# Kernel optimization log

Hardware: AMD Instinct MI355X
Metric: run time of the kernel (lower is better)

The kernel has to match this reference:

```python
import jax, jax.numpy as jnp
import numpy as np

N = 50000      # nodes
E = 800000     # directed edges (before self-loops)
FEAT = 120     # raw node feature dim
TOPO = 8       # topological feature dim
H1, D1 = 8, 8  # conv1: heads, per-head dim
C = 40         # out_channels (classes)
NEG_SLOPE = 0.2


def setup_inputs() -> dict:
    key = jax.random.key(0)
    ks = jax.random.split(key, 10)
    return {
        "x": jax.random.normal(ks[0], (N, FEAT), dtype=jnp.float32),
        "topo": jax.random.normal(ks[1], (N, TOPO), dtype=jnp.float32),
        "edge_index": jax.random.randint(ks[2], (2, E), 0, N, dtype=jnp.int32),
        "W1": jax.random.normal(ks[3], (FEAT + TOPO, H1 * D1), dtype=jnp.float32) * 0.1,
        "a_src1": jax.random.normal(ks[4], (H1, D1), dtype=jnp.float32) * 0.1,
        "a_dst1": jax.random.normal(ks[5], (H1, D1), dtype=jnp.float32) * 0.1,
        "b1": jnp.zeros((H1 * D1,), dtype=jnp.float32),
        "W2": jax.random.normal(ks[6], (H1 * D1, C), dtype=jnp.float32) * 0.1,
        "a_src2": jax.random.normal(ks[7], (1, C), dtype=jnp.float32) * 0.1,
        "a_dst2": jax.random.normal(ks[8], (1, C), dtype=jnp.float32) * 0.1,
        "b2": jnp.zeros((C,), dtype=jnp.float32),
    }


def gat_conv(x, src, dst, W, a_src, a_dst, b, heads, d, concat):
    """PyG-style GATConv (eval mode). src/dst already include self-loops."""
    n = x.shape[0]
    h = (x @ W).reshape(n, heads, d)                      # [N,H,D]
    al_src = jnp.sum(h * a_src[None], axis=-1)            # [N,H]
    al_dst = jnp.sum(h * a_dst[None], axis=-1)            # [N,H]
    e = jax.nn.leaky_relu(al_src[src] + al_dst[dst], NEG_SLOPE)  # [E',H]
    # segment softmax over incoming edges per destination node
    m = jax.ops.segment_max(e, dst, num_segments=n)       # [N,H]
    p = jnp.exp(e - m[dst])                               # [E',H]
    s = jax.ops.segment_sum(p, dst, num_segments=n)       # [N,H]
    alpha = p / s[dst]                                    # [E',H]
    out = jax.ops.segment_sum(alpha[:, :, None] * h[src], dst, num_segments=n)  # [N,H,D]
    if concat:
        return out.reshape(n, heads * d) + b
    return out.mean(axis=1) + b


def reference(x, topo, edge_index, W1, a_src1, a_dst1, b1, W2, a_src2, a_dst2, b2):
    n = x.shape[0]
    loops = jnp.arange(n, dtype=edge_index.dtype)
    src = jnp.concatenate([edge_index[0], loops])
    dst = jnp.concatenate([edge_index[1], loops])
    xin = jnp.concatenate([x, topo], axis=1)              # [N, FEAT+TOPO]
    h = jax.nn.elu(gat_conv(xin, src, dst, W1, a_src1, a_dst1, b1, H1, D1, True))
    out = gat_conv(h, src, dst, W2, a_src2, a_dst2, b2, 1, C, False)
    return jax.nn.log_softmax(out, axis=1)
```

## Files before the change

kernel.cpp:

```cpp
#include <hip/hip_runtime.h>
#include <hip/hip_fp16.h>

#define NN 50000
#define EE 800000
#define ET 850000
#define NBUCK 196
#define CAP 5120
#define TILEA 2048
#define NBA ((EE + TILEA - 1) / TILEA)
#define NGB 782

typedef _Float16 half8 __attribute__((ext_vector_type(8)));
typedef float floatx4 __attribute__((ext_vector_type(4)));

__global__ void k_zero(int* __restrict__ c) {
    int i = threadIdx.x;
    if (i < NBUCK) c[i] = 0;
}

__global__ __launch_bounds__(256) void k_bucketA(const int* __restrict__ ei,
        int* __restrict__ cursor, unsigned* __restrict__ bucketData) {
    __shared__ int cnt[NBUCK], base[NBUCK];
    int t = threadIdx.x;
    for (int i = t; i < NBUCK; i += 256) cnt[i] = 0;
    __syncthreads();
    int e0 = blockIdx.x * TILEA;
    int nE = min(TILEA, EE - e0);
    unsigned pk[8]; int bk[8], rk[8];
    int m = 0;
    for (int i = t; i < nE; i += 256) {
        int e = e0 + i;
        int s = ei[e], d = ei[EE + e];
        pk[m] = ((unsigned)d << 16) | (unsigned)s;
        bk[m] = d >> 8;
        rk[m] = atomicAdd(&cnt[bk[m]], 1);
        m++;
    }
    __syncthreads();
    for (int i = t; i < NBUCK; i += 256)
        base[i] = (cnt[i] > 0) ? atomicAdd(&cursor[i], cnt[i]) : 0;
    __syncthreads();
    for (int k = 0; k < m; k++) {
        int pos = base[bk[k]] + rk[k];
        if (pos < CAP) bucketData[(size_t)bk[k] * CAP + pos] = pk[k];
    }
}

__global__ void k_scanB(const int* __restrict__ cursor, int* __restrict__ bucketOut,
                        int* __restrict__ rowstart) {
    __shared__ int s0[256], s1[256];
    int t = threadIdx.x;
    int nloc = (t < NBUCK) ? min(256, NN - t * 256) : 0;
    int v = (t < NBUCK) ? (min(cursor[t], CAP) + nloc) : 0;
    s0[t] = v;
    __syncthreads();
    int* a = s0; int* b = s1;
    for (int off = 1; off < 256; off <<= 1) {
        int x = a[t] + ((t >= off) ? a[t - off] : 0);
        b[t] = x;
        __syncthreads();
        int* tmp = a; a = b; b = tmp;
    }
    if (t < NBUCK) bucketOut[t] = a[t] - v;
    if (t == NBUCK - 1) rowstart[NN] = a[t];
}

__global__ __launch_bounds__(256) void k_bucketB(const unsigned* __restrict__ bucketData,
        const int* __restrict__ cursor, const int* __restrict__ bucketOut,
        int* __restrict__ rowstart, int* __restrict__ srcs) {
    __shared__ int cnt[256], cur[256], sbuf[256];
    __shared__ int sorted[CAP + 256];
    int b = blockIdx.x, t = threadIdx.x;
    int nloc = min(256, NN - b * 256);
    int ecnt = min(cursor[b], CAP);
    size_t inBase = (size_t)b * CAP;
    int outBase = bucketOut[b];
    cnt[t] = (t < nloc) ? 1 : 0;
    __syncthreads();
    for (int i = t; i < ecnt; i += 256) {
        unsigned u = bucketData[inBase + i];
        atomicAdd(&cnt[(u >> 16) & 255], 1);
    }
    __syncthreads();
    int cv = cnt[t];
    sbuf[t] = cv;
    __syncthreads();
    int* a = sbuf; int* bb = cnt;
    for (int off = 1; off < 256; off <<= 1) {
        int x = a[t] + ((t >= off) ? a[t - off] : 0);
        bb[t] = x;
        __syncthreads();
        int* tmp = a; a = bb; bb = tmp;
    }
    int excl = a[t] - cv;
    __syncthreads();
    if (t < nloc) {
        rowstart[b * 256 + t] = outBase + excl;
        sorted[excl] = b * 256 + t;
        cur[t] = excl + 1;
    } else {
        cur[t] = 0;
    }
    __syncthreads();
    for (int i = t; i < ecnt; i += 256) {
        unsigned u = bucketData[inBase + i];
        int ld = (u >> 16) & 255;
        int p = atomicAdd(&cur[ld], 1);
        sorted[p] = (int)(u & 0xffffu);
    }
    __syncthreads();
    int total = ecnt + nloc;
    for (int i = t; i < total; i += 256) srcs[outBase + i] = sorted[i];
}

__global__ void k_prep(const float* __restrict__ W1, const float* __restrict__ W2,
                       _Float16* __restrict__ Bf1, _Float16* __restrict__ Bf2) {
    int tid = blockIdx.x * 256 + threadIdx.x;
    if (tid < 1024) {
        int kk = tid >> 8, ct = (tid >> 6) & 3, L = tid & 63;
        int k0 = kk * 32 + (L >> 4) * 8, col = ct * 16 + (L & 15);
        half8 v;
        #pragma unroll
        for (int j = 0; j < 8; j++) v[j] = (_Float16)W1[(k0 + j) * 64 + col];
        *(half8*)(Bf1 + ((size_t)((kk * 4 + ct) * 64 + L)) * 8) = v;
    } else if (tid < 1024 + 384) {
        int u = tid - 1024;
        int kk = u / 192, rem = u % 192;
        int ct = rem >> 6, L = rem & 63;
        int k0 = kk * 32 + (L >> 4) * 8, col = ct * 16 + (L & 15);
        half8 v;
        #pragma unroll
        for (int j = 0; j < 8; j++)
            v[j] = (col < 40) ? (_Float16)W2[(k0 + j) * 40 + col] : (_Float16)0.f;
        *(half8*)(Bf2 + ((size_t)((kk * 3 + ct) * 64 + L)) * 8) = v;
    }
}

__global__ __launch_bounds__(256) void k_gemm1(
    const float* __restrict__ x, const float* __restrict__ topo,
    const _Float16* __restrict__ Bf1,
    const float* __restrict__ a_src, const float* __restrict__ a_dst,
    __half* __restrict__ h1, float* __restrict__ alsrc, float* __restrict__ aldst) {
    int wave = threadIdx.x >> 6, lane = threadIdx.x & 63;
    int row0 = blockIdx.x * 64 + wave * 16;
    if (row0 >= NN) return;
    int g = lane >> 4, li = lane & 15;
    int myrow = row0 + li;
    half8 B[16];
    const half8* bp = (const half8*)Bf1;
    #pragma unroll
    for (int i = 0; i < 16; i++) B[i] = bp[i * 64 + lane];
    floatx4 acc[4] = {{0,0,0,0},{0,0,0,0},{0,0,0,0},{0,0,0,0}};
    #pragma unroll
    for (int kk = 0; kk < 4; kk++) {
        int k0 = kk * 32 + g * 8;
        const float* sp = (k0 == 120) ? (topo + (size_t)myrow * 8)
                                      : (x + (size_t)myrow * 120 + k0);
        float4 u0 = ((const float4*)sp)[0];
        float4 u1 = ((const float4*)sp)[1];
        half8 av;
        av[0] = (_Float16)u0.x; av[1] = (_Float16)u0.y;
        av[2] = (_Float16)u0.z; av[3] = (_Float16)u0.w;
        av[4] = (_Float16)u1.x; av[5] = (_Float16)u1.y;
        av[6] = (_Float16)u1.z; av[7] = (_Float16)u1.w;
        #pragma unroll
        for (int ct = 0; ct < 4; ct++)
            acc[ct] = __builtin_amdgcn_mfma_f32_16x16x32_f16(av, B[kk * 4 + ct], acc[ct], 0, 0, 0);
    }
    #pragma unroll
    for (int ct = 0; ct < 4; ct++)
        #pragma unroll
        for (int r = 0; r < 4; r++)
            h1[(size_t)(row0 + 4 * g + r) * 64 + ct * 16 + li] = __float2half(acc[ct][r]);
    float ps[4][4], pd[4][4];
    #pragma unroll
    for (int ct = 0; ct < 4; ct++) {
        int head = 2 * ct + (li >> 3), dix = li & 7;
        float asv = a_src[head * 8 + dix];
        float adv = a_dst[head * 8 + dix];
        #pragma unroll
        for (int r = 0; r < 4; r++) {
            ps[ct][r] = acc[ct][r] * asv;
            pd[ct][r] = acc[ct][r] * adv;
        }
    }
    #pragma unroll
    for (int off = 1; off <= 4; off <<= 1)
        #pragma unroll
        for (int ct = 0; ct < 4; ct++)
            #pragma unroll
            for (int r = 0; r < 4; r++) {
                ps[ct][r] += __shfl_xor(ps[ct][r], off, 64);
                pd[ct][r] += __shfl_xor(pd[ct][r], off, 64);
            }
    if ((li & 7) == 0) {
        #pragma unroll
        for (int ct = 0; ct < 4; ct++) {
            int head = 2 * ct + (li >> 3);
            #pragma unroll
            for (int r = 0; r < 4; r++) {
                int row = row0 + 4 * g + r;
                alsrc[row * 8 + head] = ps[ct][r];
                aldst[row * 8 + head] = pd[ct][r];
            }
        }
    }
}

__global__ __launch_bounds__(256) void k_agg1(
    const int* __restrict__ rowstart, const int* __restrict__ srcs,
    const float* __restrict__ alsrc, const float* __restrict__ aldst,
    const __half* __restrict__ h1, const float* __restrict__ b1,
    __half* __restrict__ hout) {
    int wave = threadIdx.x >> 6;
    int lane = threadIdx.x & 63;
    int d = blockIdx.x * 4 + wave;
    if (d >= NN) return;
    int half = lane >> 5;
    int cp = lane & 31;
    int h = cp >> 2;
    float adst = aldst[d * 8 + h];
    int jb = rowstart[d], je = rowstart[d + 1];
    float ssum = 0.f;
    float ax = 0.f, ay = 0.f;
    int j = jb;
    for (; j + 8 <= je; j += 8) {
        int s0 = srcs[j + half], s1 = srcs[j + 2 + half];
        int s2 = srcs[j + 4 + half], s3 = srcs[j + 6 + half];
        float e0 = alsrc[s0 * 8 + h] + adst;
        float e1 = alsrc[s1 * 8 + h] + adst;
        float e2 = alsrc[s2 * 8 + h] + adst;
        float e3 = alsrc[s3 * 8 + h] + adst;
        __half2 v0 = *(const __half2*)(h1 + (size_t)s0 * 64 + 2 * cp);
        __half2 v1 = *(const __half2*)(h1 + (size_t)s1 * 64 + 2 * cp);
        __half2 v2 = *(const __half2*)(h1 + (size_t)s2 * 64 + 2 * cp);
        __half2 v3 = *(const __half2*)(h1 + (size_t)s3 * 64 + 2 * cp);
        float p0 = __expf(fmaxf(e0, 0.2f * e0));
        float p1 = __expf(fmaxf(e1, 0.2f * e1));
        float p2 = __expf(fmaxf(e2, 0.2f * e2));
        float p3 = __expf(fmaxf(e3, 0.2f * e3));
        float2 f0 = __half22float2(v0), f1 = __half22float2(v1);
        float2 f2 = __half22float2(v2), f3 = __half22float2(v3);
        ssum += (p0 + p1) + (p2 + p3);
        ax += p0 * f0.x + p1 * f1.x + p2 * f2.x + p3 * f3.x;
        ay += p0 * f0.y + p1 * f1.y + p2 * f2.y + p3 * f3.y;
    }
    for (; j < je; j += 2) {
        int e = j + half;
        bool valid = (e < je);
        int s = srcs[valid ? e : jb];
        float ea = alsrc[s * 8 + h] + adst;
        float p = valid ? __expf(fmaxf(ea, 0.2f * ea)) : 0.f;
        float2 f = __half22float2(*(const __half2*)(h1 + (size_t)s * 64 + 2 * cp));
        ssum += p;
        ax += p * f.x;
        ay += p * f.y;
    }
    ssum += __shfl_xor(ssum, 32, 64);
    ax += __shfl_xor(ax, 32, 64);
    ay += __shfl_xor(ay, 32, 64);
    if (half == 0) {
        float2 bv = *(const float2*)(b1 + 2 * cp);
        float inv = 1.f / ssum;
        float vx = ax * inv + bv.x;
        float vy = ay * inv + bv.y;
        vx = (vx > 0.f) ? vx : (__expf(vx) - 1.f);
        vy = (vy > 0.f) ? vy : (__expf(vy) - 1.f);
        *(__half2*)(hout + (size_t)d * 64 + 2 * cp) = __floats2half2_rn(vx, vy);
    }
}

__global__ __launch_bounds__(256) void k_gemm2(
    const __half* __restrict__ hout, const _Float16* __restrict__ Bf2,
    const float* __restrict__ a_src2, const float* __restrict__ a_dst2,
    __half* __restrict__ h2, float* __restrict__ al2s, float* __restrict__ al2d) {
    int wave = threadIdx.x >> 6, lane = threadIdx.x & 63;
    int row0 = blockIdx.x * 64 + wave * 16;
    if (row0 >= NN) return;
    int g = lane >> 4, li = lane & 15;
    int myrow = row0 + li;
    half8 B[6];
    const half8* bp = (const half8*)Bf2;
    #pragma unroll
    for (int i = 0; i < 6; i++) B[i] = bp[i * 64 + lane];
    floatx4 acc[3] = {{0,0,0,0},{0,0,0,0},{0,0,0,0}};
    #pragma unroll
    for (int kk = 0; kk < 2; kk++) {
        int k0 = kk * 32 + g * 8;
        half8 av = *(const half8*)(hout + (size_t)myrow * 64 + k0);
        #pragma unroll
        for (int ct = 0; ct < 3; ct++)
            acc[ct] = __builtin_amdgcn_mfma_f32_16x16x32_f16(av, B[kk * 3 + ct], acc[ct], 0, 0, 0);
    }
    float ts[4] = {0.f, 0.f, 0.f, 0.f}, td[4] = {0.f, 0.f, 0.f, 0.f};
    #pragma unroll
    for (int ct = 0; ct < 3; ct++) {
        int col = ct * 16 + li;
        bool ok = (col < 40);
        float asv = ok ? a_src2[col] : 0.f;
        float adv = ok ? a_dst2[col] : 0.f;
        #pragma unroll
        for (int r = 0; r < 4; r++) {
            ts[r] += acc[ct][r] * asv;
            td[r] += acc[ct][r] * adv;
            if (ok) h2[(size_t)(row0 + 4 * g + r) * 40 + col] = __float2half(acc[ct][r]);
        }
    }
    #pragma unroll
    for (int off = 1; off <= 8; off <<= 1)
        #pragma unroll
        for (int r = 0; r < 4; r++) {
            ts[r] += __shfl_xor(ts[r], off, 64);
            td[r] += __shfl_xor(td[r], off, 64);
        }
    if (li == 0) {
        #pragma unroll
        for (int r = 0; r < 4; r++) {
            int row = row0 + 4 * g + r;
            al2s[row] = ts[r];
            al2d[row] = td[r];
        }
    }
}

__global__ __launch_bounds__(256) void k_agg2(
    const int* __restrict__ rowstart, const int* __restrict__ srcs,
    const float* __restrict__ al2s, const float* __restrict__ al2d,
    const __half* __restrict__ h2, const float* __restrict__ b2,
    float* __restrict__ out) {
    int wave = threadIdx.x >> 6;
    int lane = threadIdx.x & 63;
    int d = blockIdx.x * 4 + wave;
    if (d >= NN) return;
    int half = lane >> 5;
    int cp = lane & 31;
    bool act = (cp < 20);
    int cpc = act ? cp : 0;
    float adst = al2d[d];
    int jb = rowstart[d], je = rowstart[d + 1];
    float ssum = 0.f, ax = 0.f, ay = 0.f;
    int j = jb;
    for (; j + 8 <= je; j += 8) {
        int s0 = srcs[j + half], s1 = srcs[j + 2 + half];
        int s2 = srcs[j + 4 + half], s3 = srcs[j + 6 + half];
        float e0 = al2s[s0] + adst;
        float e1 = al2s[s1] + adst;
        float e2 = al2s[s2] + adst;
        float e3 = al2s[s3] + adst;
        __half2 v0 = *(const __half2*)(h2 + (size_t)s0 * 40 + 2 * cpc);
        __half2 v1 = *(const __half2*)(h2 + (size_t)s1 * 40 + 2 * cpc);
        __half2 v2 = *(const __half2*)(h2 + (size_t)s2 * 40 + 2 * cpc);
        __half2 v3 = *(const __half2*)(h2 + (size_t)s3 * 40 + 2 * cpc);
        float p0 = __expf(fmaxf(e0, 0.2f * e0));
        float p1 = __expf(fmaxf(e1, 0.2f * e1));
        float p2 = __expf(fmaxf(e2, 0.2f * e2));
        float p3 = __expf(fmaxf(e3, 0.2f * e3));
        float2 f0 = __half22float2(v0), f1 = __half22float2(v1);
        float2 f2 = __half22float2(v2), f3 = __half22float2(v3);
        ssum += (p0 + p1) + (p2 + p3);
        ax += p0 * f0.x + p1 * f1.x + p2 * f2.x + p3 * f3.x;
        ay += p0 * f0.y + p1 * f1.y + p2 * f2.y + p3 * f3.y;
    }
    for (; j < je; j += 2) {
        int e = j + half;
        bool valid = (e < je);
        int s = srcs[valid ? e : jb];
        float ea = al2s[s] + adst;
        float p = valid ? __expf(fmaxf(ea, 0.2f * ea)) : 0.f;
        float2 f = __half22float2(*(const __half2*)(h2 + (size_t)s * 40 + 2 * cpc));
        ssum += p;
        ax += p * f.x;
        ay += p * f.y;
    }
    ssum += __shfl_xor(ssum, 32, 64);
    ax += __shfl_xor(ax, 32, 64);
    ay += __shfl_xor(ay, 32, 64);
    float inv = 1.f / ssum;
    float2 bv = *(const float2*)(b2 + 2 * cpc);
    float ox = ax * inv + bv.x;
    float oy = ay * inv + bv.y;
    float mo = act ? fmaxf(ox, oy) : -3.0e38f;
    #pragma unroll
    for (int off = 16; off; off >>= 1) mo = fmaxf(mo, __shfl_xor(mo, off, 64));
    float te = act ? (__expf(ox - mo) + __expf(oy - mo)) : 0.f;
    #pragma unroll
    for (int off = 16; off; off >>= 1) te += __shfl_xor(te, off, 64);
    float ls = __logf(te);
    if (act && half == 0)
        *(float2*)(out + (size_t)d * 40 + 2 * cp) = make_float2(ox - mo - ls, oy - mo - ls);
}

extern "C" void kernel_launch(void* const* d_in, const int* in_sizes, int n_in,
                              void* d_out, int out_size, void* d_ws, size_t ws_size,
                              hipStream_t stream) {
    (void)in_sizes; (void)n_in; (void)out_size; (void)ws_size;
    const float* x    = (const float*)d_in[0];
    const float* topo = (const float*)d_in[1];
    const int*   ei   = (const int*)d_in[2];
    const float* W1   = (const float*)d_in[3];
    const float* as1  = (const float*)d_in[4];
    const float* ad1  = (const float*)d_in[5];
    const float* b1   = (const float*)d_in[6];
    const float* W2   = (const float*)d_in[7];
    const float* as2  = (const float*)d_in[8];
    const float* ad2  = (const float*)d_in[9];
    const float* b2   = (const float*)d_in[10];
    float* out = (float*)d_out;

    char* ws = (char*)d_ws;
    size_t off = 0;
    auto alloc = [&](size_t bytes) {
        void* p = ws + off;
        off += (bytes + 255) / 256 * 256;
        return p;
    };
    int*       rowstart   = (int*)alloc((NN + 1) * 4);
    int*       cursor     = (int*)alloc(NBUCK * 4);
    int*       bucketOut  = (int*)alloc(NBUCK * 4);
    unsigned*  bucketData = (unsigned*)alloc((size_t)NBUCK * CAP * 4);
    int*       srcs       = (int*)alloc(ET * 4);
    float*     alsrc1     = (float*)alloc((size_t)NN * 8 * 4);
    float*     aldst1     = (float*)alloc((size_t)NN * 8 * 4);
    float*     al2s       = (float*)alloc(NN * 4);
    float*     al2d       = (float*)alloc(NN * 4);
    _Float16*  Bf1        = (_Float16*)alloc(4 * 4 * 64 * 8 * 2);
    _Float16*  Bf2        = (_Float16*)alloc(2 * 3 * 64 * 8 * 2);
    __half*    h1         = (__half*)alloc((size_t)NN * 64 * 2);
    __half*    hout       = (__half*)alloc((size_t)NN * 64 * 2);
    __half*    h2         = h1;

    k_zero    <<<1,     256, 0, stream>>>(cursor);
    k_prep    <<<6,     256, 0, stream>>>(W1, W2, Bf1, Bf2);
    k_bucketA <<<NBA,   256, 0, stream>>>(ei, cursor, bucketData);
    k_scanB   <<<1,     256, 0, stream>>>(cursor, bucketOut, rowstart);
    k_bucketB <<<NBUCK, 256, 0, stream>>>(bucketData, cursor, bucketOut, rowstart, srcs);
    k_gemm1   <<<NGB,   256, 0, stream>>>(x, topo, Bf1, as1, ad1, h1, alsrc1, aldst1);
    k_agg1    <<<(NN + 3) / 4, 256, 0, stream>>>(rowstart, srcs, alsrc1, aldst1, h1, b1, hout);
    k_gemm2   <<<NGB,   256, 0, stream>>>(hout, Bf2, as2, ad2, h2, al2s, al2d);
    k_agg2    <<<(NN + 3) / 4, 256, 0, stream>>>(rowstart, srcs, al2s, al2d, h2, b2, out);
}
```

Before: 204.3 us.

## Fuse layer-2 GEMM into aggregation, pad CSR rows to multiples of 8

```diff
diff --git a/kernel.cpp b/kernel.cpp
--- a/kernel.cpp
+++ b/kernel.cpp
@@ -3,19 +3,33 @@
 
 #define NN 50000
 #define EE 800000
-#define ET 850000
 #define NBUCK 196
 #define CAP 5120
-#define TILEA 2048
+#define TILEA 1024
 #define NBA ((EE + TILEA - 1) / TILEA)
 #define NGB 782
+#define SRCS_MAX (EE + 8 * NN)
 
 typedef _Float16 half8 __attribute__((ext_vector_type(8)));
 typedef float floatx4 __attribute__((ext_vector_type(4)));
 
-__global__ void k_zero(int* __restrict__ c) {
-    int i = threadIdx.x;
-    if (i < NBUCK) c[i] = 0;
+__global__ void k_prep(const float* __restrict__ W1, _Float16* __restrict__ Bf1,
+                       int* __restrict__ cursor, float* __restrict__ alsrc,
+                       float* __restrict__ al2s) {
+    int tid = blockIdx.x * 256 + threadIdx.x;
+    if (tid < 1024) {
+        int kk = tid >> 8, ct = (tid >> 6) & 3, L = tid & 63;
+        int k0 = kk * 32 + (L >> 4) * 8, col = ct * 16 + (L & 15);
+        half8 v;
+        #pragma unroll
+        for (int j = 0; j < 8; j++) v[j] = (_Float16)W1[(k0 + j) * 64 + col];
+        *(half8*)(Bf1 + ((size_t)((kk * 4 + ct) * 64 + L)) * 8) = v;
+    } else {
+        int u = tid - 1024;
+        if (u < NBUCK) cursor[u] = 0;
+        if (u >= 200 && u < 208) alsrc[(size_t)NN * 8 + (u - 200)] = -1e30f;
+        if (u == 208) al2s[NN] = -1e30f;
+    }
 }
 
 __global__ __launch_bounds__(256) void k_bucketA(const int* __restrict__ ei,
@@ -26,7 +40,7 @@
     __syncthreads();
     int e0 = blockIdx.x * TILEA;
     int nE = min(TILEA, EE - e0);
-    unsigned pk[8]; int bk[8], rk[8];
+    unsigned pk[4]; int bk[4], rk[4];
     int m = 0;
     for (int i = t; i < nE; i += 256) {
         int e = e0 + i;
@@ -46,12 +60,11 @@
     }
 }
 
-__global__ void k_scanB(const int* __restrict__ cursor, int* __restrict__ bucketOut,
-                        int* __restrict__ rowstart) {
+__global__ void k_scanB(const int* __restrict__ cursor, int* __restrict__ bucketOut) {
     __shared__ int s0[256], s1[256];
     int t = threadIdx.x;
     int nloc = (t < NBUCK) ? min(256, NN - t * 256) : 0;
-    int v = (t < NBUCK) ? (min(cursor[t], CAP) + nloc) : 0;
+    int v = (t < NBUCK) ? (min(cursor[t], CAP) + 8 * nloc) : 0;
     s0[t] = v;
     __syncthreads();
     int* a = s0; int* b = s1;
@@ -62,14 +75,13 @@
         int* tmp = a; a = b; b = tmp;
     }
     if (t < NBUCK) bucketOut[t] = a[t] - v;
-    if (t == NBUCK - 1) rowstart[NN] = a[t];
 }
 
 __global__ __launch_bounds__(256) void k_bucketB(const unsigned* __restrict__ bucketData,
         const int* __restrict__ cursor, const int* __restrict__ bucketOut,
-        int* __restrict__ rowstart, int* __restrict__ srcs) {
+        int2* __restrict__ rowseg, int* __restrict__ srcs) {
     __shared__ int cnt[256], cur[256], sbuf[256];
-    __shared__ int sorted[CAP + 256];
+    __shared__ int sorted[CAP + 2048];
     int b = blockIdx.x, t = threadIdx.x;
     int nloc = min(256, NN - b * 256);
     int ecnt = min(cursor[b], CAP);
@@ -83,7 +95,8 @@
     }
     __syncthreads();
     int cv = cnt[t];
-    sbuf[t] = cv;
+    int pcv = (t < nloc) ? ((cv + 7) & ~7) : 0;
+    sbuf[t] = pcv;
     __syncthreads();
     int* a = sbuf; int* bb = cnt;
     for (int off = 1; off < 256; off <<= 1) {
@@ -92,14 +105,14 @@
         __syncthreads();
         int* tmp = a; a = bb; bb = tmp;
     }
-    int excl = a[t] - cv;
+    int excl = a[t] - pcv;
+    int total = a[255];
     __syncthreads();
     if (t < nloc) {
-        rowstart[b * 256 + t] = outBase + excl;
+        rowseg[b * 256 + t] = make_int2(outBase + excl, outBase + excl + pcv);
         sorted[excl] = b * 256 + t;
+        for (int k = cv; k < pcv; k++) sorted[excl + k] = NN;
         cur[t] = excl + 1;
-    } else {
-        cur[t] = 0;
     }
     __syncthreads();
     for (int i = t; i < ecnt; i += 256) {
@@ -109,31 +122,7 @@
         sorted[p] = (int)(u & 0xffffu);
     }
     __syncthreads();
-    int total = ecnt + nloc;
     for (int i = t; i < total; i += 256) srcs[outBase + i] = sorted[i];
-}
-
-__global__ void k_prep(const float* __restrict__ W1, const float* __restrict__ W2,
-                       _Float16* __restrict__ Bf1, _Float16* __restrict__ Bf2) {
-    int tid = blockIdx.x * 256 + threadIdx.x;
-    if (tid < 1024) {
-        int kk = tid >> 8, ct = (tid >> 6) & 3, L = tid & 63;
-        int k0 = kk * 32 + (L >> 4) * 8, col = ct * 16 + (L & 15);
-        half8 v;
-        #pragma unroll
-        for (int j = 0; j < 8; j++) v[j] = (_Float16)W1[(k0 + j) * 64 + col];
-        *(half8*)(Bf1 + ((size_t)((kk * 4 + ct) * 64 + L)) * 8) = v;
-    } else if (tid < 1024 + 384) {
-        int u = tid - 1024;
-        int kk = u / 192, rem = u % 192;
-        int ct = rem >> 6, L = rem & 63;
-        int k0 = kk * 32 + (L >> 4) * 8, col = ct * 16 + (L & 15);
-        half8 v;
-        #pragma unroll
-        for (int j = 0; j < 8; j++)
-            v[j] = (col < 40) ? (_Float16)W2[(k0 + j) * 40 + col] : (_Float16)0.f;
-        *(half8*)(Bf2 + ((size_t)((kk * 3 + ct) * 64 + L)) * 8) = v;
-    }
 }
 
 __global__ __launch_bounds__(256) void k_gemm1(
@@ -208,186 +197,149 @@
 }
 
 __global__ __launch_bounds__(256) void k_agg1(
-    const int* __restrict__ rowstart, const int* __restrict__ srcs,
+    const int2* __restrict__ rowseg, const int* __restrict__ srcs,
     const float* __restrict__ alsrc, const float* __restrict__ aldst,
     const __half* __restrict__ h1, const float* __restrict__ b1,
-    __half* __restrict__ hout) {
-    int wave = threadIdx.x >> 6;
-    int lane = threadIdx.x & 63;
-    int d = blockIdx.x * 4 + wave;
-    if (d >= NN) return;
-    int half = lane >> 5;
+    const float* __restrict__ W2, const float* __restrict__ as2g,
+    const float* __restrict__ ad2g,
+    __half* __restrict__ h2, float* __restrict__ al2s, float* __restrict__ al2d) {
+    __shared__ float W2s[64 * 40];
+    __shared__ float as2s[40], ad2s[40];
+    int t = threadIdx.x;
+    for (int i = t; i < 2560; i += 256) W2s[i] = W2[i];
+    if (t < 40) { as2s[t] = as2g[t]; ad2s[t] = ad2g[t]; }
+    __syncthreads();
+    int wave = t >> 6, lane = t & 63;
+    int hs = lane >> 5;
     int cp = lane & 31;
-    int h = cp >> 2;
-    float adst = aldst[d * 8 + h];
-    int jb = rowstart[d], je = rowstart[d + 1];
-    float ssum = 0.f;
-    float ax = 0.f, ay = 0.f;
-    int j = jb;
-    for (; j + 8 <= je; j += 8) {
-        int s0 = srcs[j + half], s1 = srcs[j + 2 + half];
-        int s2 = srcs[j + 4 + half], s3 = srcs[j + 6 + half];
-        float e0 = alsrc[s0 * 8 + h] + adst;
-        float e1 = alsrc[s1 * 8 + h] + adst;
-        float e2 = alsrc[s2 * 8 + h] + adst;
-        float e3 = alsrc[s3 * 8 + h] + adst;
-        __half2 v0 = *(const __half2*)(h1 + (size_t)s0 * 64 + 2 * cp);
-        __half2 v1 = *(const __half2*)(h1 + (size_t)s1 * 64 + 2 * cp);
-        __half2 v2 = *(const __half2*)(h1 + (size_t)s2 * 64 + 2 * cp);
-        __half2 v3 = *(const __half2*)(h1 + (size_t)s3 * 64 + 2 * cp);
-        float p0 = __expf(fmaxf(e0, 0.2f * e0));
-        float p1 = __expf(fmaxf(e1, 0.2f * e1));
-        float p2 = __expf(fmaxf(e2, 0.2f * e2));
-        float p3 = __expf(fmaxf(e3, 0.2f * e3));
-        float2 f0 = __half22float2(v0), f1 = __half22float2(v1);
-        float2 f2 = __half22float2(v2), f3 = __half22float2(v3);
-        ssum += (p0 + p1) + (p2 + p3);
-        ax += p0 * f0.x + p1 * f1.x + p2 * f2.x + p3 * f3.x;
-        ay += p0 * f0.y + p1 * f1.y + p2 * f2.y + p3 * f3.y;
-    }
-    for (; j < je; j += 2) {
-        int e = j + half;
-        bool valid = (e < je);
-        int s = srcs[valid ? e : jb];
-        float ea = alsrc[s * 8 + h] + adst;
-        float p = valid ? __expf(fmaxf(ea, 0.2f * ea)) : 0.f;
-        float2 f = __half22float2(*(const __half2*)(h1 + (size_t)s * 64 + 2 * cp));
-        ssum += p;
-        ax += p * f.x;
-        ay += p * f.y;
-    }
-    ssum += __shfl_xor(ssum, 32, 64);
-    ax += __shfl_xor(ax, 32, 64);
-    ay += __shfl_xor(ay, 32, 64);
-    if (half == 0) {
+    int hh = cp >> 2;
+    int c = lane;
+    bool ok = (c < 40);
+    int cc = ok ? c : 0;
+    for (int g = 0; g < 4; g++) {
+        int d = blockIdx.x * 16 + wave * 4 + g;
+        int2 seg = rowseg[d];
+        int jb = seg.x, je = seg.y;
+        float adst = aldst[d * 8 + hh];
+        float ssum = 0.f, ax = 0.f, ay = 0.f;
+        int sA0 = srcs[jb + hs],     sA1 = srcs[jb + 2 + hs];
+        int sA2 = srcs[jb + 4 + hs], sA3 = srcs[jb + 6 + hs];
+        for (int j = jb; j < je; j += 8) {
+            int s0 = sA0, s1 = sA1, s2 = sA2, s3 = sA3;
+            int jn = j + 8;
+            if (jn < je) {
+                sA0 = srcs[jn + hs];     sA1 = srcs[jn + 2 + hs];
+                sA2 = srcs[jn + 4 + hs]; sA3 = srcs[jn + 6 + hs];
+            }
+            float e0 = alsrc[s0 * 8 + hh] + adst;
+            float e1 = alsrc[s1 * 8 + hh] + adst;
+            float e2 = alsrc[s2 * 8 + hh] + adst;
+            float e3 = alsrc[s3 * 8 + hh] + adst;
+            __half2 v0 = *(const __half2*)(h1 + (size_t)s0 * 64 + 2 * cp);
+            __half2 v1 = *(const __half2*)(h1 + (size_t)s1 * 64 + 2 * cp);
+            __half2 v2 = *(const __half2*)(h1 + (size_t)s2 * 64 + 2 * cp);
+            __half2 v3 = *(const __half2*)(h1 + (size_t)s3 * 64 + 2 * cp);
+            float p0 = __expf(fmaxf(e0, 0.2f * e0));
+            float p1 = __expf(fmaxf(e1, 0.2f * e1));
+            float p2 = __expf(fmaxf(e2, 0.2f * e2));
+            float p3 = __expf(fmaxf(e3, 0.2f * e3));
+            float2 f0 = __half22float2(v0), f1 = __half22float2(v1);
+            float2 f2 = __half22float2(v2), f3 = __half22float2(v3);
+            ssum += (p0 + p1) + (p2 + p3);
+            ax += p0 * f0.x + p1 * f1.x + p2 * f2.x + p3 * f3.x;
+            ay += p0 * f0.y + p1 * f1.y + p2 * f2.y + p3 * f3.y;
+        }
+        ssum += __shfl_xor(ssum, 32, 64);
+        ax += __shfl_xor(ax, 32, 64);
+        ay += __shfl_xor(ay, 32, 64);
         float2 bv = *(const float2*)(b1 + 2 * cp);
         float inv = 1.f / ssum;
-        float vx = ax * inv + bv.x;
-        float vy = ay * inv + bv.y;
-        vx = (vx > 0.f) ? vx : (__expf(vx) - 1.f);
-        vy = (vy > 0.f) ? vy : (__expf(vy) - 1.f);
-        *(__half2*)(hout + (size_t)d * 64 + 2 * cp) = __floats2half2_rn(vx, vy);
-    }
-}
-
-__global__ __launch_bounds__(256) void k_gemm2(
-    const __half* __restrict__ hout, const _Float16* __restrict__ Bf2,
-    const float* __restrict__ a_src2, const float* __restrict__ a_dst2,
-    __half* __restrict__ h2, float* __restrict__ al2s, float* __restrict__ al2d) {
-    int wave = threadIdx.x >> 6, lane = threadIdx.x & 63;
-    int row0 = blockIdx.x * 64 + wave * 16;
-    if (row0 >= NN) return;
-    int g = lane >> 4, li = lane & 15;
-    int myrow = row0 + li;
-    half8 B[6];
-    const half8* bp = (const half8*)Bf2;
-    #pragma unroll
-    for (int i = 0; i < 6; i++) B[i] = bp[i * 64 + lane];
-    floatx4 acc[3] = {{0,0,0,0},{0,0,0,0},{0,0,0,0}};
-    #pragma unroll
-    for (int kk = 0; kk < 2; kk++) {
-        int k0 = kk * 32 + g * 8;
-        half8 av = *(const half8*)(hout + (size_t)myrow * 64 + k0);
-        #pragma unroll
-        for (int ct = 0; ct < 3; ct++)
-            acc[ct] = __builtin_amdgcn_mfma_f32_16x16x32_f16(av, B[kk * 3 + ct], acc[ct], 0, 0, 0);
-    }
-    float ts[4] = {0.f, 0.f, 0.f, 0.f}, td[4] = {0.f, 0.f, 0.f, 0.f};
-    #pragma unroll
-    for (int ct = 0; ct < 3; ct++) {
-        int col = ct * 16 + li;
-        bool ok = (col < 40);
-        float asv = ok ? a_src2[col] : 0.f;
-        float adv = ok ? a_dst2[col] : 0.f;
-        #pragma unroll
-        for (int r = 0; r < 4; r++) {
-            ts[r] += acc[ct][r] * asv;
-            td[r] += acc[ct][r] * adv;
-            if (ok) h2[(size_t)(row0 + 4 * g + r) * 40 + col] = __float2half(acc[ct][r]);
-        }
-    }
-    #pragma unroll
-    for (int off = 1; off <= 8; off <<= 1)
-        #pragma unroll
-        for (int r = 0; r < 4; r++) {
-            ts[r] += __shfl_xor(ts[r], off, 64);
-            td[r] += __shfl_xor(td[r], off, 64);
-        }
-    if (li == 0) {
-        #pragma unroll
-        for (int r = 0; r < 4; r++) {
-            int row = row0 + 4 * g + r;
-            al2s[row] = ts[r];
-            al2d[row] = td[r];
-        }
+        float hx = ax * inv + bv.x;
+        float hy = ay * inv + bv.y;
+        hx = (hx > 0.f) ? hx : (__expf(hx) - 1.f);
+        hy = (hy > 0.f) ? hy : (__expf(hy) - 1.f);
+        float o = 0.f;
+        #pragma unroll
+        for (int kp = 0; kp < 32; kp++) {
+            float hxk = __shfl(hx, kp, 64);
+            float hyk = __shfl(hy, kp, 64);
+            o += hxk * W2s[(2 * kp) * 40 + cc] + hyk * W2s[(2 * kp + 1) * 40 + cc];
+        }
+        float s1v = ok ? o * as2s[cc] : 0.f;
+        float s2v = ok ? o * ad2s[cc] : 0.f;
+        #pragma unroll
+        for (int off = 1; off <= 32; off <<= 1) {
+            s1v += __shfl_xor(s1v, off, 64);
+            s2v += __shfl_xor(s2v, off, 64);
+        }
+        if (lane == 0) { al2s[d] = s1v; al2d[d] = s2v; }
+        float oN = __shfl(o, lane + 1, 64);
+        if (ok && !(c & 1))
+            *(__half2*)(h2 + (size_t)d * 40 + c) = __floats2half2_rn(o, oN);
     }
 }
 
 __global__ __launch_bounds__(256) void k_agg2(
-    const int* __restrict__ rowstart, const int* __restrict__ srcs,
+    const int2* __restrict__ rowseg, const int* __restrict__ srcs,
     const float* __restrict__ al2s, const float* __restrict__ al2d,
     const __half* __restrict__ h2, const float* __restrict__ b2,
     float* __restrict__ out) {
     int wave = threadIdx.x >> 6;
     int lane = threadIdx.x & 63;
-    int d = blockIdx.x * 4 + wave;
-    if (d >= NN) return;
-    int half = lane >> 5;
+    int hs = lane >> 5;
     int cp = lane & 31;
     bool act = (cp < 20);
     int cpc = act ? cp : 0;
-    float adst = al2d[d];
-    int jb = rowstart[d], je = rowstart[d + 1];
-    float ssum = 0.f, ax = 0.f, ay = 0.f;
-    int j = jb;
-    for (; j + 8 <= je; j += 8) {
-        int s0 = srcs[j + half], s1 = srcs[j + 2 + half];
-        int s2 = srcs[j + 4 + half], s3 = srcs[j + 6 + half];
-        float e0 = al2s[s0] + adst;
-        float e1 = al2s[s1] + adst;
-        float e2 = al2s[s2] + adst;
-        float e3 = al2s[s3] + adst;
-        __half2 v0 = *(const __half2*)(h2 + (size_t)s0 * 40 + 2 * cpc);
-        __half2 v1 = *(const __half2*)(h2 + (size_t)s1 * 40 + 2 * cpc);
-        __half2 v2 = *(const __half2*)(h2 + (size_t)s2 * 40 + 2 * cpc);
-        __half2 v3 = *(const __half2*)(h2 + (size_t)s3 * 40 + 2 * cpc);
-        float p0 = __expf(fmaxf(e0, 0.2f * e0));
-        float p1 = __expf(fmaxf(e1, 0.2f * e1));
-        float p2 = __expf(fmaxf(e2, 0.2f * e2));
-        float p3 = __expf(fmaxf(e3, 0.2f * e3));
-        float2 f0 = __half22float2(v0), f1 = __half22float2(v1);
-        float2 f2 = __half22float2(v2), f3 = __half22float2(v3);
-        ssum += (p0 + p1) + (p2 + p3);
-        ax += p0 * f0.x + p1 * f1.x + p2 * f2.x + p3 * f3.x;
-        ay += p0 * f0.y + p1 * f1.y + p2 * f2.y + p3 * f3.y;
-    }
-    for (; j < je; j += 2) {
-        int e = j + half;
-        bool valid = (e < je);
-        int s = srcs[valid ? e : jb];
-        float ea = al2s[s] + adst;
-        float p = valid ? __expf(fmaxf(ea, 0.2f * ea)) : 0.f;
-        float2 f = __half22float2(*(const __half2*)(h2 + (size_t)s * 40 + 2 * cpc));
-        ssum += p;
-        ax += p * f.x;
-        ay += p * f.y;
-    }
-    ssum += __shfl_xor(ssum, 32, 64);
-    ax += __shfl_xor(ax, 32, 64);
-    ay += __shfl_xor(ay, 32, 64);
-    float inv = 1.f / ssum;
-    float2 bv = *(const float2*)(b2 + 2 * cpc);
-    float ox = ax * inv + bv.x;
-    float oy = ay * inv + bv.y;
-    float mo = act ? fmaxf(ox, oy) : -3.0e38f;
-    #pragma unroll
-    for (int off = 16; off; off >>= 1) mo = fmaxf(mo, __shfl_xor(mo, off, 64));
-    float te = act ? (__expf(ox - mo) + __expf(oy - mo)) : 0.f;
-    #pragma unroll
-    for (int off = 16; off; off >>= 1) te += __shfl_xor(te, off, 64);
-    float ls = __logf(te);
-    if (act && half == 0)
-        *(float2*)(out + (size_t)d * 40 + 2 * cp) = make_float2(ox - mo - ls, oy - mo - ls);
+    for (int g = 0; g < 4; g++) {
+        int d = blockIdx.x * 16 + wave * 4 + g;
+        int2 seg = rowseg[d];
+        int jb = seg.x, je = seg.y;
+        float adst = al2d[d];
+        float ssum = 0.f, ax = 0.f, ay = 0.f;
+        int sA0 = srcs[jb + hs],     sA1 = srcs[jb + 2 + hs];
+        int sA2 = srcs[jb + 4 + hs], sA3 = srcs[jb + 6 + hs];
+        for (int j = jb; j < je; j += 8) {
+            int s0 = sA0, s1 = sA1, s2 = sA2, s3 = sA3;
+            int jn = j + 8;
+            if (jn < je) {
+                sA0 = srcs[jn + hs];     sA1 = srcs[jn + 2 + hs];
+                sA2 = srcs[jn + 4 + hs]; sA3 = srcs[jn + 6 + hs];
+            }
+            float e0 = al2s[s0] + adst;
+            float e1 = al2s[s1] + adst;
+            float e2 = al2s[s2] + adst;
+            float e3 = al2s[s3] + adst;
+            __half2 v0 = *(const __half2*)(h2 + (size_t)s0 * 40 + 2 * cpc);
+            __half2 v1 = *(const __half2*)(h2 + (size_t)s1 * 40 + 2 * cpc);
+            __half2 v2 = *(const __half2*)(h2 + (size_t)s2 * 40 + 2 * cpc);
+            __half2 v3 = *(const __half2*)(h2 + (size_t)s3 * 40 + 2 * cpc);
+            float p0 = __expf(fmaxf(e0, 0.2f * e0));
+            float p1 = __expf(fmaxf(e1, 0.2f * e1));
+            float p2 = __expf(fmaxf(e2, 0.2f * e2));
+            float p3 = __expf(fmaxf(e3, 0.2f * e3));
+            float2 f0 = __half22float2(v0), f1 = __half22float2(v1);
+            float2 f2 = __half22float2(v2), f3 = __half22float2(v3);
+            ssum += (p0 + p1) + (p2 + p3);
+            ax += p0 * f0.x + p1 * f1.x + p2 * f2.x + p3 * f3.x;
+            ay += p0 * f0.y + p1 * f1.y + p2 * f2.y + p3 * f3.y;
+        }
+        ssum += __shfl_xor(ssum, 32, 64);
+        ax += __shfl_xor(ax, 32, 64);
+        ay += __shfl_xor(ay, 32, 64);
+        float inv = 1.f / ssum;
+        float2 bv = *(const float2*)(b2 + 2 * cpc);
+        float ox = ax * inv + bv.x;
+        float oy = ay * inv + bv.y;
+        float mo = act ? fmaxf(ox, oy) : -3.0e38f;
+        #pragma unroll
+        for (int off = 16; off; off >>= 1) mo = fmaxf(mo, __shfl_xor(mo, off, 64));
+        float te = act ? (__expf(ox - mo) + __expf(oy - mo)) : 0.f;
+        #pragma unroll
+        for (int off = 16; off; off >>= 1) te += __shfl_xor(te, off, 64);
+        float ls = __logf(te);
+        if (act && hs == 0)
+            *(float2*)(out + (size_t)d * 40 + 2 * cp) = make_float2(ox - mo - ls, oy - mo - ls);
+    }
 }
 
 extern "C" void kernel_launch(void* const* d_in, const int* in_sizes, int n_in,
@@ -414,28 +366,25 @@
         off += (bytes + 255) / 256 * 256;
         return p;
     };
-    int*       rowstart   = (int*)alloc((NN + 1) * 4);
+    int2*      rowseg     = (int2*)alloc((size_t)NN * 8);
     int*       cursor     = (int*)alloc(NBUCK * 4);
     int*       bucketOut  = (int*)alloc(NBUCK * 4);
     unsigned*  bucketData = (unsigned*)alloc((size_t)NBUCK * CAP * 4);
-    int*       srcs       = (int*)alloc(ET * 4);
-    float*     alsrc1     = (float*)alloc((size_t)NN * 8 * 4);
+    int*       srcs       = (int*)alloc((size_t)SRCS_MAX * 4);
+    float*     alsrc1     = (float*)alloc((size_t)(NN + 1) * 8 * 4);
     float*     aldst1     = (float*)alloc((size_t)NN * 8 * 4);
-    float*     al2s       = (float*)alloc(NN * 4);
+    float*     al2s       = (float*)alloc((NN + 1) * 4);
     float*     al2d       = (float*)alloc(NN * 4);
     _Float16*  Bf1        = (_Float16*)alloc(4 * 4 * 64 * 8 * 2);
-    _Float16*  Bf2        = (_Float16*)alloc(2 * 3 * 64 * 8 * 2);
-    __half*    h1         = (__half*)alloc((size_t)NN * 64 * 2);
-    __half*    hout       = (__half*)alloc((size_t)NN * 64 * 2);
-    __half*    h2         = h1;
-
-    k_zero    <<<1,     256, 0, stream>>>(cursor);
-    k_prep    <<<6,     256, 0, stream>>>(W1, W2, Bf1, Bf2);
+    __half*    h1         = (__half*)alloc((size_t)(NN + 1) * 64 * 2);
+    __half*    h2         = (__half*)alloc((size_t)(NN + 1) * 40 * 2);
+
+    k_prep    <<<5,     256, 0, stream>>>(W1, Bf1, cursor, alsrc1, al2s);
     k_bucketA <<<NBA,   256, 0, stream>>>(ei, cursor, bucketData);
-    k_scanB   <<<1,     256, 0, stream>>>(cursor, bucketOut, rowstart);
-    k_bucketB <<<NBUCK, 256, 0, stream>>>(bucketData, cursor, bucketOut, rowstart, srcs);
+    k_scanB   <<<1,     256, 0, stream>>>(cursor, bucketOut);
+    k_bucketB <<<NBUCK, 256, 0, stream>>>(bucketData, cursor, bucketOut, rowseg, srcs);
     k_gemm1   <<<NGB,   256, 0, stream>>>(x, topo, Bf1, as1, ad1, h1, alsrc1, aldst1);
-    k_agg1    <<<(NN + 3) / 4, 256, 0, stream>>>(rowstart, srcs, alsrc1, aldst1, h1, b1, hout);
-    k_gemm2   <<<NGB,   256, 0, stream>>>(hout, Bf2, as2, ad2, h2, al2s, al2d);
-    k_agg2    <<<(NN + 3) / 4, 256, 0, stream>>>(rowstart, srcs, al2s, al2d, h2, b2, out);
-}
+    k_agg1    <<<3125,  256, 0, stream>>>(rowseg, srcs, alsrc1, aldst1, h1, b1,
+                                          W2, as2, ad2, h2, al2s, al2d);
+    k_agg2    <<<3125,  256, 0, stream>>>(rowseg, srcs, al2s, al2d, h2, b2, out);
+}
```

New measurement: 242.1 us. 18.5% more time.
